# Kernel optimization log

Measured on AMD Instinct MI355X. Metric: run time of the kernel, lower is better.

## Reference

```python
import jax, jax.numpy as jnp
import numpy as np

N, T, F = 20000, 8, 128
E = 320000
H_GCN, H_CONV, H_LSTM = 32, 64, 128


def setup_inputs() -> dict:
    key = jax.random.key(0)
    ks = jax.random.split(key, 16)
    s = lambda k, shape: jax.random.normal(k, shape, dtype=jnp.float32) * 0.05
    inp = {
        'x': jax.random.normal(ks[0], (N, T, F), dtype=jnp.float32),
        'edge_index': jax.random.randint(ks[1], (2, E), 0, N, dtype=jnp.int32),
        'gcn_W': s(ks[2], (F, H_GCN)),
        'gcn_b': s(ks[3], (H_GCN,)),
        'conv_W': s(ks[4], (H_CONV, H_GCN, 2)),
        'conv_b': s(ks[5], (H_CONV,)),
        'W_ih': s(ks[6], (4 * H_LSTM, H_CONV)),
        'W_hh': s(ks[7], (4 * H_LSTM, H_LSTM)),
        'b_ih': s(ks[8], (4 * H_LSTM,)),
        'b_hh': s(ks[9], (4 * H_LSTM,)),
        'fc1_W': s(ks[10], (64, H_LSTM)),
        'fc1_b': s(ks[11], (64,)),
        'fc2_W': s(ks[12], (F, 64)),
        'fc2_b': s(ks[13], (F,)),
    }
    return inp


def _forward(x, edge_index, gcn_W, gcn_b, conv_W, conv_b, W_ih, W_hh, b_ih, b_hh, fc1_W, fc1_b, fc2_W, fc2_b):
    n = x.shape[0]
    # ---- GCNConv (PyG semantics: linear, add self-loops, sym-normalized aggregate) ----
    loops = jnp.arange(n, dtype=edge_index.dtype)
    row = jnp.concatenate([edge_index[0], loops])  # source
    col = jnp.concatenate([edge_index[1], loops])  # target
    deg = jax.ops.segment_sum(jnp.ones_like(col, dtype=x.dtype), col, num_segments=n)
    dinv = jax.lax.rsqrt(deg)  # deg >= 1 thanks to self-loops
    norm = dinv[row] * dinv[col]  # [E+N]
    h = jnp.einsum('ntf,fo->nto', x, gcn_W)  # transform once for all timesteps
    msg = h[row] * norm[:, None, None]  # [E+N, T, 32]
    agg = jax.ops.segment_sum(msg, col, num_segments=n) + gcn_b
    g = jax.nn.relu(agg)  # [N, T, 32]; dropout is identity at inference
    # ---- Conv1d(32->64, k=2) over time ----
    xc = jnp.transpose(g, (0, 2, 1))  # [N, 32, T]
    y = jax.lax.conv_general_dilated(xc, conv_W, window_strides=(1,), padding='VALID',
                                     dimension_numbers=('NCH', 'OIH', 'NCH'))
    y = jax.nn.relu(y + conv_b[None, :, None])  # [N, 64, T-1]
    seq = jnp.transpose(y, (2, 0, 1))  # [T-1, N, 64]
    # ---- LSTM (torch gate order i, f, g, o) ----
    def step(carry, xt):
        hp, cp = carry
        z = xt @ W_ih.T + hp @ W_hh.T + (b_ih + b_hh)  # [N, 4H]
        i, f, gg, o = jnp.split(z, 4, axis=-1)
        c = jax.nn.sigmoid(f) * cp + jax.nn.sigmoid(i) * jnp.tanh(gg)
        hn = jax.nn.sigmoid(o) * jnp.tanh(c)
        return (hn, c), None
    h0 = jnp.zeros((n, H_LSTM), dtype=x.dtype)
    (hT, _), _ = jax.lax.scan(step, (h0, h0), seq)
    # ---- Head ----
    out = jax.nn.relu(hT @ fc1_W.T + fc1_b)
    out = jax.nn.sigmoid(out @ fc2_W.T + fc2_b)
    return out  # [N, num_features]


def reference(x, edge_index, gcn_W, gcn_b, conv_W, conv_b, W_ih, W_hh, b_ih, b_hh, fc1_W, fc1_b, fc2_W, fc2_b):
    return _forward(x, edge_index, gcn_W, gcn_b, conv_W, conv_b, W_ih, W_hh, b_ih, b_hh, fc1_W, fc1_b, fc2_W, fc2_b)
```

## Files before the change

### kernel.cpp

```cpp
#include <hip/hip_runtime.h>
#include <hip/hip_bf16.h>

#define T_STEPS 8
#define F_IN    128
#define H_GCN   32
#define H_CONV  64
#define H_LSTM  128

typedef __bf16 bf16x8 __attribute__((ext_vector_type(8)));
typedef float  f32x4  __attribute__((ext_vector_type(4)));
typedef unsigned short ushort8v __attribute__((ext_vector_type(8)));

#if __has_builtin(__builtin_amdgcn_exp2f)
__device__ __forceinline__ float exp2_f(float x) { return __builtin_amdgcn_exp2f(x); }
#else
__device__ __forceinline__ float exp2_f(float x) { return exp2f(x); }
#endif
#if __has_builtin(__builtin_amdgcn_rcpf)
__device__ __forceinline__ float rcp_f(float x) { return __builtin_amdgcn_rcpf(x); }
#else
__device__ __forceinline__ float rcp_f(float x) { return 1.f / x; }
#endif

#define NL2E  (-1.442695041f)
#define NL2E2 (-2.885390082f)

__device__ __forceinline__ float sigm_fast(float x) {
  return rcp_f(1.f + exp2_f(x * NL2E));
}

__device__ __forceinline__ float ubf(unsigned short u) {
  union { unsigned int i; float f; } v; v.i = ((unsigned int)u) << 16; return v.f;
}
__device__ __forceinline__ unsigned short bfb(float f) {
  __hip_bfloat16 b = __float2bfloat16(f);
  return __builtin_bit_cast(unsigned short, b);
}

__device__ __forceinline__ bf16x8 load_bf8(const __hip_bfloat16* p) {
  int4 v = *reinterpret_cast<const int4*>(p);
  return __builtin_bit_cast(bf16x8, v);
}

#define PREP_TOT (512*192 + 64*128 + 128*64 + 64*64 + 32*128 + 512)

__global__ __launch_bounds__(256) void k_transform(const float* __restrict__ x,
                                                   const __hip_bfloat16* __restrict__ Wgt,
                                                   const float* __restrict__ dinv,
                                                   __hip_bfloat16* __restrict__ hs)
{
  int tid  = threadIdx.x;
  int wave = tid >> 6;
  int lane = tid & 63;
  int l15  = lane & 15;
  int lhi  = lane >> 4;
  long r0  = (long)blockIdx.x * 64 + wave * 16;

  bf16x8 bw[2][4];
  #pragma unroll
  for (int ct = 0; ct < 2; ++ct)
    #pragma unroll
    for (int ks = 0; ks < 4; ++ks)
      bw[ct][ks] = load_bf8(Wgt + (ct * 16 + l15) * 128 + ks * 32 + lhi * 8);

  const float* xp = x + (r0 + l15) * 128 + lhi * 8;
  f32x4 acc[2];
  acc[0] = (f32x4){0.f, 0.f, 0.f, 0.f};
  acc[1] = (f32x4){0.f, 0.f, 0.f, 0.f};

  #pragma unroll
  for (int ks = 0; ks < 4; ++ks) {
    float4 v0 = *reinterpret_cast<const float4*>(xp + ks * 32);
    float4 v1 = *reinterpret_cast<const float4*>(xp + ks * 32 + 4);
    bf16x8 a;
    a[0] = (__bf16)v0.x; a[1] = (__bf16)v0.y; a[2] = (__bf16)v0.z; a[3] = (__bf16)v0.w;
    a[4] = (__bf16)v1.x; a[5] = (__bf16)v1.y; a[6] = (__bf16)v1.z; a[7] = (__bf16)v1.w;
    acc[0] = __builtin_amdgcn_mfma_f32_16x16x32_bf16(a, bw[0][ks], acc[0], 0, 0, 0);
    acc[1] = __builtin_amdgcn_mfma_f32_16x16x32_bf16(a, bw[1][ks], acc[1], 0, 0, 0);
  }

  #pragma unroll
  for (int r = 0; r < 4; ++r) {
    long rr = r0 + lhi * 4 + r;
    float dv = dinv[rr >> 3];
    hs[rr * 32 + l15]      = __float2bfloat16(acc[0][r] * dv);
    hs[rr * 32 + 16 + l15] = __float2bfloat16(acc[1][r] * dv);
  }
}

__global__ __launch_bounds__(256) void k_prep_count(
    const int* __restrict__ col, int* __restrict__ cnt, int E,
    const float* __restrict__ Wih, const float* __restrict__ Whh,
    const float* __restrict__ bih, const float* __restrict__ bhh,
    const float* __restrict__ fc1W, const float* __restrict__ fc2W,
    const float* __restrict__ convW, const float* __restrict__ gcnW,
    __hip_bfloat16* __restrict__ Wcat, float* __restrict__ bias,
    __hip_bfloat16* __restrict__ W1b, __hip_bfloat16* __restrict__ W2b,
    __hip_bfloat16* __restrict__ Wcb, __hip_bfloat16* __restrict__ Wgt,
    unsigned int* __restrict__ hz)
{
  int i = blockIdx.x * 256 + threadIdx.x;
  if (i < E) atomicAdd(&cnt[col[i]], 1);
  if (i < 128) hz[i] = 0u;
  if (i < 512 * 192) {
    int q = i / 192, k = i - q * 192;
    float v = (k < 64) ? Wih[q * 64 + k] : Whh[q * 128 + (k - 64)];
    Wcat[i] = __float2bfloat16(v);
  } else if (i < 512 * 192 + 64 * 128) {
    int j = i - 512 * 192;
    W1b[j] = __float2bfloat16(fc1W[j]);
  } else if (i < 512 * 192 + 64 * 128 + 128 * 64) {
    int j = i - 512 * 192 - 64 * 128;
    W2b[j] = __float2bfloat16(fc2W[j]);
  } else if (i < 512 * 192 + 64 * 128 + 128 * 64 + 64 * 64) {
    int j = i - 512 * 192 - 64 * 128 - 128 * 64;
    Wcb[j] = __float2bfloat16(convW[j]);
  } else if (i < 512 * 192 + 64 * 128 + 128 * 64 + 64 * 64 + 32 * 128) {
    int j = i - 512 * 192 - 64 * 128 - 128 * 64 - 64 * 64;
    int o = j >> 7, f = j & 127;
    Wgt[j] = __float2bfloat16(gcnW[f * 32 + o]);
  } else if (i < PREP_TOT) {
    int j = i - (PREP_TOT - 512);
    bias[j] = bih[j] + bhh[j];
  }
}

__global__ __launch_bounds__(1024) void k_scan(const int* __restrict__ cnt,
                                               int* __restrict__ row_ptr,
                                               int* __restrict__ cursor,
                                               float* __restrict__ dinv, int N)
{
  __shared__ int s[1024];
  int tid = threadIdx.x;
  const int CH = (N + 1023) >> 10;
  int i0 = tid * CH;
  int sum = 0;
  for (int j = 0; j < CH; ++j) {
    int i = i0 + j;
    if (i < N) sum += cnt[i];
  }
  s[tid] = sum;
  __syncthreads();
  #pragma unroll
  for (int off = 1; off < 1024; off <<= 1) {
    int t = (tid >= off) ? s[tid - off] : 0;
    __syncthreads();
    s[tid] += t;
    __syncthreads();
  }
  int run = (tid > 0) ? s[tid - 1] : 0;
  for (int j = 0; j < CH; ++j) {
    int i = i0 + j;
    if (i < N) {
      int v = cnt[i];
      cursor[i] = run;
      row_ptr[i] = run;
      dinv[i] = rsqrtf((float)v + 1.0f);
      run += v;
      if (i == N - 1) row_ptr[N] = run;
    }
  }
}

__global__ void k_fill(const int* __restrict__ ei, int* __restrict__ cursor,
                       int* __restrict__ adj, int E)
{
  int e = blockIdx.x * 256 + threadIdx.x;
  if (e < E) {
    int r = ei[e], c = ei[E + e];
    int pos = atomicAdd(&cursor[c], 1);
    adj[pos] = r;
  }
}

__device__ __forceinline__ void gat16(const int* __restrict__ adj, int base, int end, int NN,
                                      const __hip_bfloat16* __restrict__ hl,
                                      float& a0, float& a1, float& a2, float& a3)
{
  int lim = end - base;
  int s0 = adj[base + 0],  s1 = adj[base + 1],  s2 = adj[base + 2],  s3 = adj[base + 3];
  int s4 = adj[base + 4],  s5 = adj[base + 5],  s6 = adj[base + 6],  s7 = adj[base + 7];
  int s8 = adj[base + 8],  s9 = adj[base + 9],  sa = adj[base + 10], sb = adj[base + 11];
  int sc = adj[base + 12], sd = adj[base + 13], se = adj[base + 14], sf = adj[base + 15];
  s0 = (0  < lim) ? s0 : NN;  s1 = (1  < lim) ? s1 : NN;
  s2 = (2  < lim) ? s2 : NN;  s3 = (3  < lim) ? s3 : NN;
  s4 = (4  < lim) ? s4 : NN;  s5 = (5  < lim) ? s5 : NN;
  s6 = (6  < lim) ? s6 : NN;  s7 = (7  < lim) ? s7 : NN;
  s8 = (8  < lim) ? s8 : NN;  s9 = (9  < lim) ? s9 : NN;
  sa = (10 < lim) ? sa : NN;  sb = (11 < lim) ? sb : NN;
  sc = (12 < lim) ? sc : NN;  sd = (13 < lim) ? sd : NN;
  se = (14 < lim) ? se : NN;  sf = (15 < lim) ? sf : NN;
  ushort4 r0 = *reinterpret_cast<const ushort4*>(hl + (size_t)s0 * 256);
  ushort4 r1 = *reinterpret_cast<const ushort4*>(hl + (size_t)s1 * 256);
  ushort4 r2 = *reinterpret_cast<const ushort4*>(hl + (size_t)s2 * 256);
  ushort4 r3 = *reinterpret_cast<const ushort4*>(hl + (size_t)s3 * 256);
  ushort4 r4 = *reinterpret_cast<const ushort4*>(hl + (size_t)s4 * 256);
  ushort4 r5 = *reinterpret_cast<const ushort4*>(hl + (size_t)s5 * 256);
  ushort4 r6 = *reinterpret_cast<const ushort4*>(hl + (size_t)s6 * 256);
  ushort4 r7 = *reinterpret_cast<const ushort4*>(hl + (size_t)s7 * 256);
  ushort4 r8 = *reinterpret_cast<const ushort4*>(hl + (size_t)s8 * 256);
  ushort4 r9 = *reinterpret_cast<const ushort4*>(hl + (size_t)s9 * 256);
  ushort4 ra = *reinterpret_cast<const ushort4*>(hl + (size_t)sa * 256);
  ushort4 rb = *reinterpret_cast<const ushort4*>(hl + (size_t)sb * 256);
  ushort4 rc = *reinterpret_cast<const ushort4*>(hl + (size_t)sc * 256);
  ushort4 rd = *reinterpret_cast<const ushort4*>(hl + (size_t)sd * 256);
  ushort4 re = *reinterpret_cast<const ushort4*>(hl + (size_t)se * 256);
  ushort4 rf = *reinterpret_cast<const ushort4*>(hl + (size_t)sf * 256);
  a0 += ((ubf(r0.x) + ubf(r1.x)) + (ubf(r2.x) + ubf(r3.x))) + ((ubf(r4.x) + ubf(r5.x)) + (ubf(r6.x) + ubf(r7.x)))
      + ((ubf(r8.x) + ubf(r9.x)) + (ubf(ra.x) + ubf(rb.x))) + ((ubf(rc.x) + ubf(rd.x)) + (ubf(re.x) + ubf(rf.x)));
  a1 += ((ubf(r0.y) + ubf(r1.y)) + (ubf(r2.y) + ubf(r3.y))) + ((ubf(r4.y) + ubf(r5.y)) + (ubf(r6.y) + ubf(r7.y)))
      + ((ubf(r8.y) + ubf(r9.y)) + (ubf(ra.y) + ubf(rb.y))) + ((ubf(rc.y) + ubf(rd.y)) + (ubf(re.y) + ubf(rf.y)));
  a2 += ((ubf(r0.z) + ubf(r1.z)) + (ubf(r2.z) + ubf(r3.z))) + ((ubf(r4.z) + ubf(r5.z)) + (ubf(r6.z) + ubf(r7.z)))
      + ((ubf(r8.z) + ubf(r9.z)) + (ubf(ra.z) + ubf(rb.z))) + ((ubf(rc.z) + ubf(rd.z)) + (ubf(re.z) + ubf(rf.z)));
  a3 += ((ubf(r0.w) + ubf(r1.w)) + (ubf(r2.w) + ubf(r3.w))) + ((ubf(r4.w) + ubf(r5.w)) + (ubf(r6.w) + ubf(r7.w)))
      + ((ubf(r8.w) + ubf(r9.w)) + (ubf(ra.w) + ubf(rb.w))) + ((ubf(rc.w) + ubf(rd.w)) + (ubf(re.w) + ubf(rf.w)));
}

__global__ __launch_bounds__(256) void k_gather_conv(
    const int* __restrict__ row_ptr, const int* __restrict__ adj,
    const float* __restrict__ dinv, const __hip_bfloat16* __restrict__ hs,
    const float* __restrict__ gcnb,
    const __hip_bfloat16* __restrict__ Wcb, const float* __restrict__ bc,
    __hip_bfloat16* __restrict__ seq, int N)
{
  __shared__ __hip_bfloat16 g_lds[8 * 256];
  __shared__ __hip_bfloat16 A[4][16][72];
  int tid  = threadIdx.x;
  int wave = tid >> 6;
  int lane = tid & 63;
  int l15  = lane & 15;
  int lhi  = lane >> 4;

  if (tid < 144) {
    int w = tid / 36, q = tid % 36;
    int row = 14 + q / 18, cc = (q % 18) * 4;
    *reinterpret_cast<uint2*>(&A[w][row][cc]) = make_uint2(0u, 0u);
  }

  int na = blockIdx.x * 8 + wave * 2;
  int nb = na + 1;
  int pa = row_ptr[na], ea = row_ptr[na + 1];
  int pb = row_ptr[nb], eb = row_ptr[nb + 1];
  float da = dinv[na], db = dinv[nb];

  const __hip_bfloat16* hl = hs + lane * 4;
  float a0, a1, a2, a3, b0, b1, b2, b3;
  {
    ushort4 hva = *reinterpret_cast<const ushort4*>(hl + (size_t)na * 256);
    ushort4 hvb = *reinterpret_cast<const ushort4*>(hl + (size_t)nb * 256);
    a0 = ubf(hva.x); a1 = ubf(hva.y); a2 = ubf(hva.z); a3 = ubf(hva.w);
    b0 = ubf(hvb.x); b1 = ubf(hvb.y); b2 = ubf(hvb.z); b3 = ubf(hvb.w);
  }

  while (pa < ea && pb < eb) {
    gat16(adj, pa, ea, N, hl, a0, a1, a2, a3);
    gat16(adj, pb, eb, N, hl, b0, b1, b2, b3);
    pa += 16; pb += 16;
  }
  while (pa < ea) { gat16(adj, pa, ea, N, hl, a0, a1, a2, a3); pa += 16; }
  while (pb < eb) { gat16(adj, pb, eb, N, hl, b0, b1, b2, b3); pb += 16; }

  int ci0 = (lane * 4) & 31;
  float g0 = gcnb[ci0 + 0], g1 = gcnb[ci0 + 1], g2 = gcnb[ci0 + 2], g3 = gcnb[ci0 + 3];
  ushort4 oa, ob;
  oa.x = bfb(fmaxf(fmaf(a0, da, g0), 0.f));
  oa.y = bfb(fmaxf(fmaf(a1, da, g1), 0.f));
  oa.z = bfb(fmaxf(fmaf(a2, da, g2), 0.f));
  oa.w = bfb(fmaxf(fmaf(a3, da, g3), 0.f));
  ob.x = bfb(fmaxf(fmaf(b0, db, g0), 0.f));
  ob.y = bfb(fmaxf(fmaf(b1, db, g1), 0.f));
  ob.z = bfb(fmaxf(fmaf(b2, db, g2), 0.f));
  ob.w = bfb(fmaxf(fmaf(b3, db, g3), 0.f));
  *reinterpret_cast<ushort4*>(&g_lds[(wave * 2 + 0) * 256 + lane * 4]) = oa;
  *reinterpret_cast<ushort4*>(&g_lds[(wave * 2 + 1) * 256 + lane * 4]) = ob;
  __syncthreads();

  {
    int f0 = tid * 8;
    ushort8v v = *reinterpret_cast<const ushort8v*>(&g_lds[f0]);
    int n_local = f0 >> 8;
    int rem     = f0 & 255;
    int t_row   = rem >> 5;
    int ci      = rem & 31;
    int w       = n_local >> 1;
    int rbase   = (n_local & 1) * 7;
    #pragma unroll
    for (int e = 0; e < 8; ++e) {
      unsigned short u = v[e];
      int k0 = (ci + e) * 2;
      if (t_row <= 6)
        *reinterpret_cast<unsigned short*>(&A[w][rbase + t_row][k0]) = u;
      if (t_row >= 1)
        *reinterpret_cast<unsigned short*>(&A[w][rbase + t_row - 1][k0 + 1]) = u;
    }
  }
  __syncthreads();

  bf16x8 bfr[2][4];
  #pragma unroll
  for (int ks = 0; ks < 2; ++ks)
    #pragma unroll
    for (int cg = 0; cg < 4; ++cg)
      bfr[ks][cg] = load_bf8(Wcb + (cg * 16 + l15) * 64 + ks * 32 + lhi * 8);

  f32x4 acc[4];
  #pragma unroll
  for (int cg = 0; cg < 4; ++cg) acc[cg] = (f32x4){0.f, 0.f, 0.f, 0.f};

  #pragma unroll
  for (int ks = 0; ks < 2; ++ks) {
    bf16x8 a = load_bf8(&A[wave][l15][ks * 32 + lhi * 8]);
    #pragma unroll
    for (int cg = 0; cg < 4; ++cg)
      acc[cg] = __builtin_amdgcn_mfma_f32_16x16x32_bf16(a, bfr[ks][cg], acc[cg], 0, 0, 0);
  }

  long n64 = (long)N * 64;
  #pragma unroll
  for (int r = 0; r < 4; ++r) {
    int rr = lhi * 4 + r;
    if (rr < 14) {
      int hi = rr >= 7 ? 1 : 0;
      int nl = wave * 2 + hi;
      int t  = rr - 7 * hi;
      long n = (long)blockIdx.x * 8 + nl;
      #pragma unroll
      for (int cg = 0; cg < 4; ++cg) {
        int co = cg * 16 + l15;
        seq[(long)t * n64 + n * 64 + co] = __float2bfloat16(fmaxf(acc[cg][r] + bc[co], 0.f));
      }
    }
  }
}

__global__ __launch_bounds__(512, 2) void k_lstm_head(
    const __hip_bfloat16* __restrict__ seq,
    const __hip_bfloat16* __restrict__ Wcat,
    const float* __restrict__ bias,
    const __hip_bfloat16* __restrict__ W1b,
    const float* __restrict__ fc1b,
    const __hip_bfloat16* __restrict__ W2b,
    const float* __restrict__ fc2b,
    float* __restrict__ out, int N)
{
  __shared__ __hip_bfloat16 h_lds[2][80][136];
  __shared__ __hip_bfloat16 s1_lds[80][72];
  int tid  = threadIdx.x;
  int wave = tid >> 6;
  int lane = tid & 63;
  int l15  = lane & 15;
  int lhi  = lane >> 4;
  long n0  = (long)blockIdx.x * 80;
  int hc   = wave * 16 + l15;

  bf16x8 bw[6][4];
  #pragma unroll
  for (int ks = 0; ks < 6; ++ks)
    #pragma unroll
    for (int gg = 0; gg < 4; ++gg)
      bw[ks][gg] = load_bf8(Wcat + (size_t)(gg * 128 + hc) * 192 + ks * 32 + lhi * 8);

  float kbi = bias[hc]       * NL2E;
  float kbf = bias[128 + hc] * NL2E;
  float kbg = bias[256 + hc] * NL2E2;
  float kbo = bias[384 + hc] * NL2E;
  float c[5][4];
  #pragma unroll
  for (int g = 0; g < 5; ++g)
    #pragma unroll
    for (int r = 0; r < 4; ++r) c[g][r] = 0.f;

  size_t tstr = (size_t)N * 64;
  const __hip_bfloat16* spb = seq + (n0 + l15) * 64 + lhi * 8;

  for (int t = 0; t < 7; ++t) {
    f32x4 acc[5][4];
    #pragma unroll
    for (int g = 0; g < 5; ++g)
      #pragma unroll
      for (int gg = 0; gg < 4; ++gg)
        acc[g][gg] = (f32x4){0.f, 0.f, 0.f, 0.f};

    #pragma unroll
    for (int g = 0; g < 5; ++g) {
      const __hip_bfloat16* sp = spb + (size_t)t * tstr + (size_t)g * 16 * 64;
      bf16x8 a0 = load_bf8(sp);
      bf16x8 a1 = load_bf8(sp + 32);
      #pragma unroll
      for (int gg = 0; gg < 4; ++gg)
        acc[g][gg] = __builtin_amdgcn_mfma_f32_16x16x32_bf16(a0, bw[0][gg], acc[g][gg], 0, 0, 0);
      #pragma unroll
      for (int gg = 0; gg < 4; ++gg)
        acc[g][gg] = __builtin_amdgcn_mfma_f32_16x16x32_bf16(a1, bw[1][gg], acc[g][gg], 0, 0, 0);
    }

    if (t > 0) {
      const __hip_bfloat16* hb = &h_lds[(t + 1) & 1][0][0];
      #pragma unroll
      for (int ks = 2; ks < 6; ++ks) {
        #pragma unroll
        for (int g = 0; g < 5; ++g) {
          bf16x8 a = load_bf8(hb + (g * 16 + l15) * 136 + (ks - 2) * 32 + lhi * 8);
          #pragma unroll
          for (int gg = 0; gg < 4; ++gg)
            acc[g][gg] = __builtin_amdgcn_mfma_f32_16x16x32_bf16(a, bw[ks][gg], acc[g][gg], 0, 0, 0);
        }
      }
    }

    __hip_bfloat16* hw = &h_lds[t & 1][0][0];
    #pragma unroll
    for (int g = 0; g < 5; ++g) {
      #pragma unroll
      for (int r = 0; r < 4; ++r) {
        float si  = rcp_f(1.f + exp2_f(fmaf(acc[g][0][r], NL2E,  kbi)));
        float sf  = rcp_f(1.f + exp2_f(fmaf(acc[g][1][r], NL2E,  kbf)));
        float sg2 = rcp_f(1.f + exp2_f(fmaf(acc[g][2][r], NL2E2, kbg)));
        float so  = rcp_f(1.f + exp2_f(fmaf(acc[g][3][r], NL2E,  kbo)));
        float tg  = fmaf(2.f, sg2, -1.f);
        float cn  = fmaf(sf, c[g][r], si * tg);
        c[g][r] = cn;
        float sc2 = rcp_f(1.f + exp2_f(cn * NL2E2));
        hw[(g * 16 + lhi * 4 + r) * 136 + hc] = __float2bfloat16(so * fmaf(2.f, sc2, -1.f));
      }
    }
    __syncthreads();
  }

  if (wave < 4) {
    int col1 = wave * 16 + l15;
    float b1 = fc1b[col1];
    #pragma unroll
    for (int g = 0; g < 5; ++g) {
      f32x4 acc1v = (f32x4){0.f, 0.f, 0.f, 0.f};
      #pragma unroll
      for (int ks = 0; ks < 4; ++ks) {
        int kb = ks * 32 + lhi * 8;
        bf16x8 a = load_bf8(&h_lds[0][g * 16 + l15][kb]);
        bf16x8 b = load_bf8(W1b + col1 * 128 + kb);
        acc1v = __builtin_amdgcn_mfma_f32_16x16x32_bf16(a, b, acc1v, 0, 0, 0);
      }
      #pragma unroll
      for (int r = 0; r < 4; ++r)
        s1_lds[g * 16 + lhi * 4 + r][col1] = __float2bfloat16(fmaxf(acc1v[r] + b1, 0.f));
    }
  }
  __syncthreads();

  {
    int c2 = wave * 16 + l15;
    float b2 = fc2b[c2];
    #pragma unroll
    for (int g = 0; g < 5; ++g) {
      f32x4 acc2 = (f32x4){0.f, 0.f, 0.f, 0.f};
      #pragma unroll
      for (int ks = 0; ks < 2; ++ks) {
        int kb = ks * 32 + lhi * 8;
        bf16x8 a = load_bf8(&s1_lds[g * 16 + l15][kb]);
        bf16x8 b = load_bf8(W2b + c2 * 64 + kb);
        acc2 = __builtin_amdgcn_mfma_f32_16x16x32_bf16(a, b, acc2, 0, 0, 0);
      }
      #pragma unroll
      for (int r = 0; r < 4; ++r)
        out[(n0 + g * 16 + lhi * 4 + r) * 128 + c2] = sigm_fast(acc2[r] + b2);
    }
  }
}

extern "C" void kernel_launch(void* const* d_in, const int* in_sizes, int n_in,
                              void* d_out, int out_size, void* d_ws, size_t ws_size,
                              hipStream_t stream)
{
  const float* x     = (const float*)d_in[0];
  const int*   ei    = (const int*)d_in[1];
  const float* gcnW  = (const float*)d_in[2];
  const float* gcnb  = (const float*)d_in[3];
  const float* convW = (const float*)d_in[4];
  const float* convb = (const float*)d_in[5];
  const float* Wih   = (const float*)d_in[6];
  const float* Whh   = (const float*)d_in[7];
  const float* bih   = (const float*)d_in[8];
  const float* bhh   = (const float*)d_in[9];
  const float* fc1W  = (const float*)d_in[10];
  const float* fc1b  = (const float*)d_in[11];
  const float* fc2W  = (const float*)d_in[12];
  const float* fc2b  = (const float*)d_in[13];

  const int N = in_sizes[0] / (T_STEPS * F_IN);
  const int E = in_sizes[1] / 2;

  char* ws = (char*)d_ws;
  size_t off = 0;
  auto alloc = [&](size_t bytes) {
    void* p = ws + off;
    off = (off + bytes + 255) & ~(size_t)255;
    return p;
  };
  __hip_bfloat16* hs  = (__hip_bfloat16*)alloc((size_t)(N + 1) * 256 * 2);
  __hip_bfloat16* seq = (__hip_bfloat16*)alloc((size_t)7 * N * 64 * 2);
  int* cnt     = (int*)alloc((size_t)N * 4);
  int* row_ptr = (int*)alloc((size_t)(N + 1) * 4);
  int* cursor  = (int*)alloc((size_t)N * 4);
  float* dinv  = (float*)alloc((size_t)N * 4);
  int* adj     = (int*)alloc((size_t)(E + 16) * 4);
  __hip_bfloat16* Wcat = (__hip_bfloat16*)alloc(512 * 192 * 2);
  float* bias = (float*)alloc(512 * 4);
  __hip_bfloat16* W1b = (__hip_bfloat16*)alloc(64 * 128 * 2);
  __hip_bfloat16* W2b = (__hip_bfloat16*)alloc(128 * 64 * 2);
  __hip_bfloat16* Wcb = (__hip_bfloat16*)alloc(64 * 64 * 2);
  __hip_bfloat16* Wgt = (__hip_bfloat16*)alloc(32 * 128 * 2);

  hipMemsetAsync(cnt, 0, (size_t)N * 4, stream);

  int pc_work = E > PREP_TOT ? E : PREP_TOT;
  k_prep_count<<<(pc_work + 255) / 256, 256, 0, stream>>>(
      ei + E, cnt, E, Wih, Whh, bih, bhh, fc1W, fc2W, convW, gcnW,
      Wcat, bias, W1b, W2b, Wcb, Wgt, (unsigned int*)(hs + (size_t)N * 256));
  k_scan<<<1, 1024, 0, stream>>>(cnt, row_ptr, cursor, dinv, N);
  k_transform<<<(N * T_STEPS) / 64, 256, 0, stream>>>(x, Wgt, dinv, hs);
  k_fill<<<(E + 255) / 256, 256, 0, stream>>>(ei, cursor, adj, E);
  k_gather_conv<<<N / 8, 256, 0, stream>>>(row_ptr, adj, dinv, hs, gcnb, Wcb, convb, seq, N);
  k_lstm_head<<<N / 80, 512, 0, stream>>>(seq, Wcat, bias, W1b, fc1b, W2b, fc2b, (float*)d_out, N);
}
```

Before: 201.5 us.

## Fuse edge fill into transform kernel and use wave-shuffle prefix scan

Merges the CSR adjacency fill into the GCN feature-transform kernel, which removes one launch and lets the atomic scatter overlap with the MFMA transform work. The grid is N*T/64 = 2500 blocks of 256 threads, enough to cover E edges. The single-block scan now loads counts with vector loads, scans with wave shuffles plus a small cross-wave pass instead of a 10-step shared-memory scan, and writes its outputs with vector stores. The count buffer and outputs are padded to make the vector accesses safe, and each thread now holds up to 32 counts in registers.

```diff
diff --git a/kernel.cpp b/kernel.cpp
--- a/kernel.cpp
+++ b/kernel.cpp
@@ -44,12 +44,25 @@
 
 #define PREP_TOT (512*192 + 64*128 + 128*64 + 64*64 + 32*128 + 512)
 
-__global__ __launch_bounds__(256) void k_transform(const float* __restrict__ x,
-                                                   const __hip_bfloat16* __restrict__ Wgt,
-                                                   const float* __restrict__ dinv,
-                                                   __hip_bfloat16* __restrict__ hs)
+__global__ __launch_bounds__(256) void k_transform_fill(
+    const float* __restrict__ x,
+    const __hip_bfloat16* __restrict__ Wgt,
+    const float* __restrict__ dinv,
+    __hip_bfloat16* __restrict__ hs,
+    const int* __restrict__ ei, int* __restrict__ cursor,
+    int* __restrict__ adj, int E)
 {
   int tid  = threadIdx.x;
+
+  {
+    int e = blockIdx.x * 256 + tid;
+    if (e < E) {
+      int r = ei[e], ctg = ei[E + e];
+      int pos = atomicAdd(&cursor[ctg], 1);
+      adj[pos] = r;
+    }
+  }
+
   int wave = tid >> 6;
   int lane = tid & 63;
   int l15  = lane & 15;
@@ -130,46 +143,70 @@
                                                int* __restrict__ cursor,
                                                float* __restrict__ dinv, int N)
 {
-  __shared__ int s[1024];
-  int tid = threadIdx.x;
+  __shared__ int wsum[16];
+  int tid  = threadIdx.x;
+  int lane = tid & 63;
+  int wid  = tid >> 6;
   const int CH = (N + 1023) >> 10;
+  const int nv = (CH + 3) >> 2;
   int i0 = tid * CH;
+
+  int vals[32];
+  #pragma unroll
+  for (int q = 0; q < 8; ++q) {
+    if (q < nv) {
+      int4 v = *reinterpret_cast<const int4*>(cnt + i0 + q * 4);
+      vals[q * 4 + 0] = v.x; vals[q * 4 + 1] = v.y;
+      vals[q * 4 + 2] = v.z; vals[q * 4 + 3] = v.w;
+    }
+  }
   int sum = 0;
-  for (int j = 0; j < CH; ++j) {
-    int i = i0 + j;
-    if (i < N) sum += cnt[i];
-  }
-  s[tid] = sum;
+  #pragma unroll
+  for (int j = 0; j < 32; ++j) if (j < CH) sum += vals[j];
+
+  int v = sum;
+  #pragma unroll
+  for (int off = 1; off < 64; off <<= 1) {
+    int t = __shfl_up(v, off);
+    if (lane >= off) v += t;
+  }
+  if (lane == 63) wsum[wid] = v;
   __syncthreads();
-  #pragma unroll
-  for (int off = 1; off < 1024; off <<= 1) {
-    int t = (tid >= off) ? s[tid - off] : 0;
-    __syncthreads();
-    s[tid] += t;
-    __syncthreads();
-  }
-  int run = (tid > 0) ? s[tid - 1] : 0;
-  for (int j = 0; j < CH; ++j) {
-    int i = i0 + j;
-    if (i < N) {
-      int v = cnt[i];
-      cursor[i] = run;
-      row_ptr[i] = run;
-      dinv[i] = rsqrtf((float)v + 1.0f);
-      run += v;
-      if (i == N - 1) row_ptr[N] = run;
-    }
-  }
-}
-
-__global__ void k_fill(const int* __restrict__ ei, int* __restrict__ cursor,
-                       int* __restrict__ adj, int E)
-{
-  int e = blockIdx.x * 256 + threadIdx.x;
-  if (e < E) {
-    int r = ei[e], c = ei[E + e];
-    int pos = atomicAdd(&cursor[c], 1);
-    adj[pos] = r;
+  if (wid == 0) {
+    int w = (lane < 16) ? wsum[lane] : 0;
+    #pragma unroll
+    for (int off = 1; off < 16; off <<= 1) {
+      int t = __shfl_up(w, off);
+      if (lane >= off) w += t;
+    }
+    if (lane < 16) wsum[lane] = w;
+  }
+  __syncthreads();
+
+  int run = v - sum + ((wid > 0) ? wsum[wid - 1] : 0);
+  if (i0 < N) {
+    int rp[32], cu[32]; float dv[32];
+    #pragma unroll
+    for (int q = 0; q < 32; ++q) {
+      if (q < CH) {
+        int c = vals[q];
+        rp[q] = run; cu[q] = run;
+        dv[q] = rsqrtf((float)c + 1.0f);
+        run += c;
+      }
+    }
+    #pragma unroll
+    for (int q = 0; q < 8; ++q) {
+      if (q < nv) {
+        *reinterpret_cast<int4*>(row_ptr + i0 + q * 4) =
+            make_int4(rp[q*4], rp[q*4+1], rp[q*4+2], rp[q*4+3]);
+        *reinterpret_cast<int4*>(cursor + i0 + q * 4) =
+            make_int4(cu[q*4], cu[q*4+1], cu[q*4+2], cu[q*4+3]);
+        *reinterpret_cast<float4*>(dinv + i0 + q * 4) =
+            make_float4(dv[q*4], dv[q*4+1], dv[q*4+2], dv[q*4+3]);
+      }
+    }
+    if (i0 + CH >= N) row_ptr[N] = run;
   }
 }
 
@@ -488,6 +525,8 @@
 
   const int N = in_sizes[0] / (T_STEPS * F_IN);
   const int E = in_sizes[1] / 2;
+  const int CH = (N + 1023) >> 10;
+  const int cntPad = 1024 * CH;
 
   char* ws = (char*)d_ws;
   size_t off = 0;
@@ -498,10 +537,10 @@
   };
   __hip_bfloat16* hs  = (__hip_bfloat16*)alloc((size_t)(N + 1) * 256 * 2);
   __hip_bfloat16* seq = (__hip_bfloat16*)alloc((size_t)7 * N * 64 * 2);
-  int* cnt     = (int*)alloc((size_t)N * 4);
-  int* row_ptr = (int*)alloc((size_t)(N + 1) * 4);
-  int* cursor  = (int*)alloc((size_t)N * 4);
-  float* dinv  = (float*)alloc((size_t)N * 4);
+  int* cnt     = (int*)alloc((size_t)cntPad * 4);
+  int* row_ptr = (int*)alloc((size_t)(N + 4) * 4);
+  int* cursor  = (int*)alloc((size_t)(N + 4) * 4);
+  float* dinv  = (float*)alloc((size_t)(N + 4) * 4);
   int* adj     = (int*)alloc((size_t)(E + 16) * 4);
   __hip_bfloat16* Wcat = (__hip_bfloat16*)alloc(512 * 192 * 2);
   float* bias = (float*)alloc(512 * 4);
@@ -510,15 +549,14 @@
   __hip_bfloat16* Wcb = (__hip_bfloat16*)alloc(64 * 64 * 2);
   __hip_bfloat16* Wgt = (__hip_bfloat16*)alloc(32 * 128 * 2);
 
-  hipMemsetAsync(cnt, 0, (size_t)N * 4, stream);
+  hipMemsetAsync(cnt, 0, (size_t)cntPad * 4, stream);
 
   int pc_work = E > PREP_TOT ? E : PREP_TOT;
   k_prep_count<<<(pc_work + 255) / 256, 256, 0, stream>>>(
       ei + E, cnt, E, Wih, Whh, bih, bhh, fc1W, fc2W, convW, gcnW,
       Wcat, bias, W1b, W2b, Wcb, Wgt, (unsigned int*)(hs + (size_t)N * 256));
   k_scan<<<1, 1024, 0, stream>>>(cnt, row_ptr, cursor, dinv, N);
-  k_transform<<<(N * T_STEPS) / 64, 256, 0, stream>>>(x, Wgt, dinv, hs);
-  k_fill<<<(E + 255) / 256, 256, 0, stream>>>(ei, cursor, adj, E);
+  k_transform_fill<<<(N * T_STEPS) / 64, 256, 0, stream>>>(x, Wgt, dinv, hs, ei, cursor, adj, E);
   k_gather_conv<<<N / 8, 256, 0, stream>>>(row_ptr, adj, dinv, hs, gcnb, Wcb, convb, seq, N);
   k_lstm_head<<<N / 80, 512, 0, stream>>>(seq, Wcat, bias, W1b, fc1b, W2b, fc2b, (float*)d_out, N);
 }
```

Result: slower. 490.8 us (+143.6%).
